# Kernel optimization log

Hardware: AMD Instinct MI355X
Metric: run time of the kernel (lower is better)

The kernel has to match this reference:

```python
import jax, jax.numpy as jnp
import numpy as np
import math

B, D, S, H = 4, 1024, 2048, 16


def setup_inputs() -> dict:
    key = jax.random.key(0)
    ks = jax.random.split(key, 9)
    scale = 0.02
    return {
        "x": jax.random.normal(ks[0], (B, D, S), dtype=jnp.float32),
        "Wq": jax.random.normal(ks[1], (D, D), dtype=jnp.float32) * scale,
        "bq": jnp.zeros((D,), dtype=jnp.float32),
        "Wk": jax.random.normal(ks[2], (D, D), dtype=jnp.float32) * scale,
        "bk": jnp.zeros((D,), dtype=jnp.float32),
        "Wv": jax.random.normal(ks[3], (D, D), dtype=jnp.float32) * scale,
        "bv": jnp.zeros((D,), dtype=jnp.float32),
        "Wo": jax.random.normal(ks[4], (D, D), dtype=jnp.float32) * scale,
        "bo": jnp.zeros((D,), dtype=jnp.float32),
        "num_heads": H,
    }


def _positional_encoding(d_model, seq_len):
    # pe[0::2, :] = sin(pos * denom), pe[1::2, :] = cos(pos * denom)
    pos = jnp.arange(seq_len, dtype=jnp.float32)[None, :]            # [1, S]
    denom = jnp.exp(jnp.arange(0, d_model, 2, dtype=jnp.float32)
                    * (-math.log(10000.0) / d_model))[:, None]        # [D/2, 1]
    angles = pos * denom                                              # [D/2, S]
    pe = jnp.zeros((d_model, seq_len), dtype=jnp.float32)
    pe = pe.at[0::2, :].set(jnp.sin(angles))
    pe = pe.at[1::2, :].set(jnp.cos(angles))
    return pe


def reference(x, Wq, bq, Wk, bk, Wv, bv, Wo, bo, num_heads):
    b, d_model, s = x.shape
    head_dim = d_model // num_heads
    x = x + _positional_encoding(d_model, s)[None, :, :]  # broadcast over batch
    x = jnp.transpose(x, (0, 2, 1))                       # [B, S, D]
    q = x @ Wq.T + bq
    k = x @ Wk.T + bk
    v = x @ Wv.T + bv
    # [B, S, H, hd] -> [B, H, S, hd]
    q = q.reshape(b, s, num_heads, head_dim).transpose(0, 2, 1, 3)
    k = k.reshape(b, s, num_heads, head_dim).transpose(0, 2, 1, 3)
    v = v.reshape(b, s, num_heads, head_dim).transpose(0, 2, 1, 3)
    scores = jnp.einsum('bhqd,bhkd->bhqk', q, k) / jnp.sqrt(
        jnp.asarray(head_dim, dtype=jnp.float32))
    attn = jax.nn.softmax(scores, axis=-1)
    out = jnp.einsum('bhqk,bhkd->bhqd', attn, v)          # [B, H, S, hd]
    out = out.transpose(0, 2, 1, 3).reshape(b, s, d_model)
    out = out @ Wo.T + bo
    return jnp.transpose(out, (0, 2, 1))                  # [B, D, S]
```

## Files before the change

kernel.cpp:

```cpp
#include <hip/hip_runtime.h>


typedef __bf16 bf16;
typedef __attribute__((ext_vector_type(8))) __bf16 bf16x8;
typedef __attribute__((ext_vector_type(4))) __bf16 bf16x4;
typedef __attribute__((ext_vector_type(4))) float f32x4;

#define NB 4
#define ND 1024
#define NS 2048
#define NH 16
#define NM 8192

__device__ __forceinline__ void gld16(const void* g, void* l) {
  __builtin_amdgcn_global_load_lds((__attribute__((address_space(1))) void*)g,
                                   (__attribute__((address_space(3))) void*)l, 16, 0, 0);
}

__device__ __forceinline__ float exp2_fast(float x) {
#if __has_builtin(__builtin_amdgcn_exp2f)
  return __builtin_amdgcn_exp2f(x);
#else
  return exp2f(x);
#endif
}

__global__ __launch_bounds__(256) void prep_x_kernel(const float* __restrict__ x,
                                                     bf16* __restrict__ xT) {
  __shared__ float t[32][33];
  const int tx = threadIdx.x, ty = threadIdx.y;
  const int s0 = blockIdx.x * 32, d0 = blockIdx.y * 32, b = blockIdx.z;
#pragma unroll
  for (int i = 0; i < 4; ++i) {
    const int rr = ty + i * 8;
    const int d = d0 + rr, s = s0 + tx;
    const float freq = __expf(-(float)(d >> 1) * 0.01798894603980689f);
    const float ang = (float)s * freq;
    const float pe = (d & 1) ? cosf(ang) : sinf(ang);
    t[rr][tx] = x[((size_t)b * ND + d) * NS + s] + pe;
  }
  __syncthreads();
#pragma unroll
  for (int i = 0; i < 4; ++i) {
    const int a = ty + i * 8;
    xT[((size_t)b * NS + s0 + a) * ND + d0 + tx] = (bf16)t[tx][a];
  }
}

__global__ __launch_bounds__(256) void prep_w_kernel(const float* __restrict__ Wq,
                                                     const float* __restrict__ Wk,
                                                     const float* __restrict__ Wv,
                                                     const float* __restrict__ Wo,
                                                     bf16* __restrict__ Wqkv,
                                                     bf16* __restrict__ WoB) {
  const size_t t = (size_t)blockIdx.x * blockDim.x + threadIdx.x;
  const size_t i = t * 4;
  const float* src;
  bf16* dst;
  size_t off;
  if (i < (size_t)3 * 1024 * 1024) {
    const int sel = (int)(i >> 20);
    src = sel == 0 ? Wq : (sel == 1 ? Wk : Wv);
    off = i - ((size_t)sel << 20);
    dst = Wqkv + i;
  } else {
    src = Wo;
    off = i - ((size_t)3 << 20);
    dst = WoB + off;
  }
  const f32x4 v = *(const f32x4*)(src + off);
  bf16x4 o;
  o[0] = (bf16)v[0];
  o[1] = (bf16)v[1];
  o[2] = (bf16)v[2];
  o[3] = (bf16)v[3];
  *(bf16x4*)dst = o;
}

__device__ __forceinline__ void gemm_tile_128(const bf16* __restrict__ A,
                                              const bf16* __restrict__ Bm,
                                              int tm, int tn, bf16* ldsA, bf16* ldsB,
                                              f32x4 acc[4][4]) {
  const int tid = threadIdx.x;
  const int lane = tid & 63, wave = tid >> 6;
  const int wm = wave >> 1, wn = wave & 1;
  const int rl = lane & 15, quad = lane >> 4;
  int r0[4], c0[4];
#pragma unroll
  for (int j = 0; j < 4; ++j) {
    const int o = (wave * 4 + j) * 1024 + lane * 16;
    const int r = o >> 7;
    r0[j] = r;
    c0[j] = ((((o >> 4) & 7) ^ (r & 7)) * 8);
  }
  for (int kt = 0; kt < 1024; kt += 64) {
#pragma unroll
    for (int j = 0; j < 4; ++j) {
      gld16(A + (size_t)(tm + r0[j]) * 1024 + kt + c0[j], (char*)ldsA + (wave * 4 + j) * 1024);
      gld16(Bm + (size_t)(tn + r0[j]) * 1024 + kt + c0[j], (char*)ldsB + (wave * 4 + j) * 1024);
    }
    __syncthreads();
#pragma unroll
    for (int kk = 0; kk < 2; ++kk) {
      bf16x8 af[4], bfr[4];
#pragma unroll
      for (int i = 0; i < 4; ++i) {
        const int ra = wm * 64 + i * 16 + rl;
        af[i] = *(const bf16x8*)((const char*)ldsA + ra * 128 +
                                 (((kk * 4 + quad) ^ (rl & 7)) * 16));
        const int rb = wn * 64 + i * 16 + rl;
        bfr[i] = *(const bf16x8*)((const char*)ldsB + rb * 128 +
                                  (((kk * 4 + quad) ^ (rl & 7)) * 16));
      }
#pragma unroll
      for (int i = 0; i < 4; ++i)
#pragma unroll
        for (int j = 0; j < 4; ++j)
          acc[i][j] =
              __builtin_amdgcn_mfma_f32_16x16x32_bf16(af[i], bfr[j], acc[i][j], 0, 0, 0);
    }
    __syncthreads();
  }
}

__global__ __launch_bounds__(256, 2) void gemm_qkv_kernel(
    const bf16* __restrict__ xT, const bf16* __restrict__ Wqkv,
    const float* __restrict__ bq, const float* __restrict__ bk,
    const float* __restrict__ bv, bf16* __restrict__ Q, bf16* __restrict__ Kb,
    bf16* __restrict__ VT) {
  __shared__ bf16 ldsA[128 * 64], ldsB[128 * 64];
  const int tm = blockIdx.x * 128, tn = blockIdx.y * 128;
  f32x4 acc[4][4];
  const f32x4 z = {0.f, 0.f, 0.f, 0.f};
#pragma unroll
  for (int i = 0; i < 4; ++i)
#pragma unroll
    for (int j = 0; j < 4; ++j) acc[i][j] = z;
  gemm_tile_128(xT, Wqkv, tm, tn, ldsA, ldsB, acc);
  const int lane = threadIdx.x & 63, wave = threadIdx.x >> 6;
  const int wm = wave >> 1, wn = wave & 1;
  const int rl = lane & 15, quad = lane >> 4;
  const float QSCALE = 0.18033688011112042f;
#pragma unroll
  for (int j = 0; j < 4; ++j) {
    const int n = tn + wn * 64 + j * 16 + rl;
    const int which = n >> 10;
    const int nl = n & 1023;
    const int h = nl >> 6, d = nl & 63;
    const float bias = (which == 0 ? bq : which == 1 ? bk : bv)[nl];
#pragma unroll
    for (int i = 0; i < 4; ++i) {
      const int m0 = tm + wm * 64 + i * 16 + quad * 4;
      const int b = m0 >> 11, s0 = m0 & 2047;
      const size_t bh = (size_t)(b * 16 + h);
      if (which == 2) {
        bf16x4 pk;
#pragma unroll
        for (int r = 0; r < 4; ++r) pk[r] = (bf16)(acc[i][j][r] + bias);
        *(bf16x4*)(VT + ((size_t)bh * 64 + d) * 2048 + s0) = pk;
      } else {
#pragma unroll
        for (int r = 0; r < 4; ++r) {
          const float v = acc[i][j][r] + bias;
          const int s = s0 + r;
          if (which == 0)
            Q[(bh * 2048 + s) * 64 + d] = (bf16)(v * QSCALE);
          else
            Kb[(bh * 2048 + s) * 64 + d] = (bf16)v;
        }
      }
    }
  }
}

__global__ __launch_bounds__(256, 2) void attn_kernel(const bf16* __restrict__ Q,
                                                      const bf16* __restrict__ Kb,
                                                      const bf16* __restrict__ VT,
                                                      bf16* __restrict__ AO) {
  __shared__ __align__(16) char smem[65536];
  char* ldsK = smem;
  char* ldsV = smem + 16384;
  char* ldsP = smem + 32768;
  const int tid = threadIdx.x;
  const int lane = tid & 63, wave = tid >> 6;
  const int rl = lane & 15, quad = lane >> 4;
  const int bh = blockIdx.x;
  const int q0 = blockIdx.y * 256;
  const bf16* Qb = Q + ((size_t)bh * 2048 + q0) * 64;
  const bf16* Kbb = Kb + (size_t)bh * 2048 * 64;
  const bf16* Vb = VT + (size_t)bh * 64 * 2048;
  const int o0 = wave * 1024 + lane * 16, o1 = o0 + 4096;
  const int ra = o0 >> 7, rb = o1 >> 7;
  const int ca = (((o0 >> 4) & 7) ^ (ra & 7)) * 16;
  const int cb = (((o1 >> 4) & 7) ^ (rb & 7)) * 16;
  gld16((const char*)Kbb + (size_t)ra * 128 + ca, ldsK + wave * 1024);
  gld16((const char*)Kbb + (size_t)rb * 128 + cb, ldsK + wave * 1024 + 4096);
  gld16((const char*)Vb + (size_t)ra * 4096 + ca, ldsV + wave * 1024);
  gld16((const char*)Vb + (size_t)rb * 4096 + cb, ldsV + wave * 1024 + 4096);
  bf16x8 qf[4][2];
#pragma unroll
  for (int i = 0; i < 4; ++i)
#pragma unroll
    for (int ks = 0; ks < 2; ++ks)
      qf[i][ks] =
          *(const bf16x8*)(Qb + (wave * 64 + i * 16 + rl) * 64 + ks * 32 + quad * 8);
  f32x4 o_acc[4][4], lacc[4];
  const f32x4 z = {0.f, 0.f, 0.f, 0.f};
#pragma unroll
  for (int i = 0; i < 4; ++i) {
    lacc[i] = z;
#pragma unroll
    for (int j = 0; j < 4; ++j) o_acc[i][j] = z;
  }
  const bf16 oneb = (bf16)1.0f;
  const bf16x8 onesb = {oneb, oneb, oneb, oneb, oneb, oneb, oneb, oneb};
  char* Pw = ldsP + wave * 8192;
  int buf = 0;
  for (int kt = 0; kt < 2048; kt += 64, buf ^= 1) {
    __syncthreads();
    if (kt + 64 < 2048) {
      const int nb = (buf ^ 1) * 8192;
      gld16((const char*)Kbb + (size_t)(kt + 64 + ra) * 128 + ca, ldsK + nb + wave * 1024);
      gld16((const char*)Kbb + (size_t)(kt + 64 + rb) * 128 + cb,
            ldsK + nb + wave * 1024 + 4096);
      gld16((const char*)Vb + (size_t)ra * 4096 + (size_t)(kt + 64) * 2 + ca,
            ldsV + nb + wave * 1024);
      gld16((const char*)Vb + (size_t)rb * 4096 + (size_t)(kt + 64) * 2 + cb,
            ldsV + nb + wave * 1024 + 4096);
    }
    const char* Kbase = ldsK + buf * 8192;
    const char* Vbase = ldsV + buf * 8192;
#pragma unroll
    for (int jk = 0; jk < 4; ++jk) {
      const bf16x8 kf0 =
          *(const bf16x8*)(Kbase + (jk * 16 + rl) * 128 + ((quad ^ (rl & 7)) * 16));
      const bf16x8 kf1 =
          *(const bf16x8*)(Kbase + (jk * 16 + rl) * 128 + (((4 + quad) ^ (rl & 7)) * 16));
#pragma unroll
      for (int i = 0; i < 4; ++i) {
        f32x4 s = z;
        s = __builtin_amdgcn_mfma_f32_16x16x32_bf16(kf0, qf[i][0], s, 0, 0, 0);
        s = __builtin_amdgcn_mfma_f32_16x16x32_bf16(kf1, qf[i][1], s, 0, 0, 0);
        bf16x4 pk;
#pragma unroll
        for (int r = 0; r < 4; ++r) pk[r] = (bf16)exp2_fast(s[r]);
        *(bf16x4*)(Pw + (i * 16 + rl) * 128 + (((jk * 2 + (quad >> 1)) ^ (rl & 7)) * 16) +
                   (quad & 1) * 8) = pk;
      }
    }
    asm volatile("s_waitcnt lgkmcnt(0)" ::: "memory");
#pragma unroll
    for (int ks = 0; ks < 2; ++ks) {
      bf16x8 pf[4];
#pragma unroll
      for (int i = 0; i < 4; ++i)
        pf[i] = *(const bf16x8*)(Pw + (i * 16 + rl) * 128 +
                                 (((ks * 4 + quad) ^ (rl & 7)) * 16));
#pragma unroll
      for (int i = 0; i < 4; ++i)
        lacc[i] = __builtin_amdgcn_mfma_f32_16x16x32_bf16(pf[i], onesb, lacc[i], 0, 0, 0);
#pragma unroll
      for (int j = 0; j < 4; ++j) {
        const bf16x8 vf = *(const bf16x8*)(Vbase + (j * 16 + rl) * 128 +
                                           (((ks * 4 + quad) ^ (rl & 7)) * 16));
#pragma unroll
        for (int i = 0; i < 4; ++i)
          o_acc[i][j] =
              __builtin_amdgcn_mfma_f32_16x16x32_bf16(pf[i], vf, o_acc[i][j], 0, 0, 0);
      }
    }
  }
  const int b = bh >> 4, h = bh & 15;
#pragma unroll
  for (int i = 0; i < 4; ++i) {
    f32x4 linv;
#pragma unroll
    for (int r = 0; r < 4; ++r) linv[r] = __builtin_amdgcn_rcpf(lacc[i][r]);
#pragma unroll
    for (int j = 0; j < 4; ++j)
#pragma unroll
      for (int r = 0; r < 4; ++r) {
        const int s = q0 + wave * 64 + i * 16 + quad * 4 + r;
        const int d = h * 64 + j * 16 + rl;
        AO[((size_t)b * 2048 + s) * 1024 + d] = (bf16)(o_acc[i][j][r] * linv[r]);
      }
  }
}

__global__ __launch_bounds__(256, 2) void gemm_out_kernel(const bf16* __restrict__ AO,
                                                          const bf16* __restrict__ WoB,
                                                          const float* __restrict__ bo,
                                                          float* __restrict__ out) {
  __shared__ bf16 ldsA[128 * 64], ldsB[128 * 64];
  const int tm = blockIdx.x * 128, tn = blockIdx.y * 128;
  f32x4 acc[4][4];
  const f32x4 z = {0.f, 0.f, 0.f, 0.f};
#pragma unroll
  for (int i = 0; i < 4; ++i)
#pragma unroll
    for (int j = 0; j < 4; ++j) acc[i][j] = z;
  gemm_tile_128(AO, WoB, tm, tn, ldsA, ldsB, acc);
  const int lane = threadIdx.x & 63, wave = threadIdx.x >> 6;
  const int wm = wave >> 1, wn = wave & 1;
  const int rl = lane & 15, quad = lane >> 4;
#pragma unroll
  for (int j = 0; j < 4; ++j) {
    const int n = tn + wn * 64 + j * 16 + rl;
    const float bias = bo[n];
#pragma unroll
    for (int i = 0; i < 4; ++i) {
      const int m0 = tm + wm * 64 + i * 16 + quad * 4;
      const int b = m0 >> 11, s = m0 & 2047;
      f32x4 v = acc[i][j];
      v[0] += bias;
      v[1] += bias;
      v[2] += bias;
      v[3] += bias;
      *(f32x4*)(out + ((size_t)(b * 1024 + n)) * 2048 + s) = v;
    }
  }
}

extern "C" void kernel_launch(void* const* d_in, const int* in_sizes, int n_in,
                              void* d_out, int out_size, void* d_ws, size_t ws_size,
                              hipStream_t stream) {
  const float* x = (const float*)d_in[0];
  const float* Wq = (const float*)d_in[1];
  const float* bq = (const float*)d_in[2];
  const float* Wk = (const float*)d_in[3];
  const float* bk = (const float*)d_in[4];
  const float* Wv = (const float*)d_in[5];
  const float* bv = (const float*)d_in[6];
  const float* Wo = (const float*)d_in[7];
  const float* bo = (const float*)d_in[8];
  float* out = (float*)d_out;

  char* p = (char*)d_ws;
  bf16* xT = (bf16*)p;
  p += (size_t)NM * ND * 2;
  bf16* Wqkv = (bf16*)p;
  p += (size_t)3 * ND * ND * 2;
  bf16* WoB = (bf16*)p;
  p += (size_t)ND * ND * 2;
  bf16* Qb = (bf16*)p;
  p += (size_t)NM * ND * 2;
  bf16* Kbf = (bf16*)p;
  p += (size_t)NM * ND * 2;
  bf16* VTb = (bf16*)p;
  p += (size_t)NM * ND * 2;
  bf16* AO = xT;

  prep_x_kernel<<<dim3(NS / 32, ND / 32, NB), dim3(32, 8), 0, stream>>>(x, xT);
  prep_w_kernel<<<dim3(4096), dim3(256), 0, stream>>>(Wq, Wk, Wv, Wo, Wqkv, WoB);
  gemm_qkv_kernel<<<dim3(NM / 128, 3072 / 128), dim3(256), 0, stream>>>(
      xT, Wqkv, bq, bk, bv, Qb, Kbf, VTb);
  attn_kernel<<<dim3(NB * NH, NS / 256), dim3(256), 0, stream>>>(Qb, Kbf, VTb, AO);
  gemm_out_kernel<<<dim3(NM / 128, ND / 128), dim3(256), 0, stream>>>(AO, WoB, bo, out);
}
```

Baseline: 278.9 us.

## Keep attention P in registers via permlane swaps and halve query tile

The attention kernel no longer writes exp'd scores to LDS and reads them back as MFMA A-operands. It builds the P fragments in registers using permlane32/permlane16 swaps, with a shuffle fallback. This drops the 32KB P buffer and the lgkmcnt wait. The query tile per block is halved to 128 rows (32 per wave) and launch bounds are raised to 4 blocks per CU, aiming for higher occupancy with less LDS. The trade-off is that K/V tiles are reloaded by twice as many blocks, and each wave does less MFMA work per K/V load.

```diff
diff --git a/kernel.cpp b/kernel.cpp
--- a/kernel.cpp
+++ b/kernel.cpp
@@ -4,7 +4,10 @@
 typedef __bf16 bf16;
 typedef __attribute__((ext_vector_type(8))) __bf16 bf16x8;
 typedef __attribute__((ext_vector_type(4))) __bf16 bf16x4;
+typedef __attribute__((ext_vector_type(2))) __bf16 bf16x2;
 typedef __attribute__((ext_vector_type(4))) float f32x4;
+typedef __attribute__((ext_vector_type(2))) unsigned int uintx2;
+typedef __attribute__((ext_vector_type(4))) unsigned int uintx4;
 
 #define NB 4
 #define ND 1024
@@ -22,6 +25,33 @@
   return __builtin_amdgcn_exp2f(x);
 #else
   return exp2f(x);
+#endif
+}
+
+__device__ __forceinline__ unsigned pk2(float a, float b) {
+  bf16x2 t;
+  t[0] = (bf16)a;
+  t[1] = (bf16)b;
+  return __builtin_bit_cast(unsigned int, t);
+}
+
+__device__ __forceinline__ void lane_xchg(unsigned a, unsigned b, unsigned& lo,
+                                          unsigned& hi) {
+#if __has_builtin(__builtin_amdgcn_permlane32_swap) && \
+    __has_builtin(__builtin_amdgcn_permlane16_swap)
+  uintx2 r = __builtin_amdgcn_permlane32_swap(a, b, false, false);
+  uintx2 r2 = __builtin_amdgcn_permlane16_swap(r[0], r[1], false, false);
+  lo = r2[0];
+  hi = r2[1];
+#else
+  const int lane = threadIdx.x & 63;
+  const int src = (lane & 15) + ((lane >> 4) & 1) * 32;
+  const unsigned as = (unsigned)__shfl((int)a, src, 64);
+  const unsigned bs = (unsigned)__shfl((int)b, src, 64);
+  const unsigned as2 = (unsigned)__shfl((int)a, src + 16, 64);
+  const unsigned bs2 = (unsigned)__shfl((int)b, src + 16, 64);
+  lo = (lane >= 32) ? bs : as;
+  hi = (lane >= 32) ? bs2 : as2;
 #endif
 }
 
@@ -173,19 +203,18 @@
   }
 }
 
-__global__ __launch_bounds__(256, 2) void attn_kernel(const bf16* __restrict__ Q,
+__global__ __launch_bounds__(256, 4) void attn_kernel(const bf16* __restrict__ Q,
                                                       const bf16* __restrict__ Kb,
                                                       const bf16* __restrict__ VT,
                                                       bf16* __restrict__ AO) {
-  __shared__ __align__(16) char smem[65536];
+  __shared__ __align__(16) char smem[32768];
   char* ldsK = smem;
   char* ldsV = smem + 16384;
-  char* ldsP = smem + 32768;
   const int tid = threadIdx.x;
   const int lane = tid & 63, wave = tid >> 6;
   const int rl = lane & 15, quad = lane >> 4;
   const int bh = blockIdx.x;
-  const int q0 = blockIdx.y * 256;
+  const int q0 = blockIdx.y * 128;
   const bf16* Qb = Q + ((size_t)bh * 2048 + q0) * 64;
   const bf16* Kbb = Kb + (size_t)bh * 2048 * 64;
   const bf16* Vb = VT + (size_t)bh * 64 * 2048;
@@ -197,24 +226,23 @@
   gld16((const char*)Kbb + (size_t)rb * 128 + cb, ldsK + wave * 1024 + 4096);
   gld16((const char*)Vb + (size_t)ra * 4096 + ca, ldsV + wave * 1024);
   gld16((const char*)Vb + (size_t)rb * 4096 + cb, ldsV + wave * 1024 + 4096);
-  bf16x8 qf[4][2];
-#pragma unroll
-  for (int i = 0; i < 4; ++i)
+  bf16x8 qf[2][2];
+#pragma unroll
+  for (int i = 0; i < 2; ++i)
 #pragma unroll
     for (int ks = 0; ks < 2; ++ks)
       qf[i][ks] =
-          *(const bf16x8*)(Qb + (wave * 64 + i * 16 + rl) * 64 + ks * 32 + quad * 8);
-  f32x4 o_acc[4][4], lacc[4];
+          *(const bf16x8*)(Qb + (wave * 32 + i * 16 + rl) * 64 + ks * 32 + quad * 8);
+  f32x4 o_acc[2][4], lacc[2];
   const f32x4 z = {0.f, 0.f, 0.f, 0.f};
 #pragma unroll
-  for (int i = 0; i < 4; ++i) {
+  for (int i = 0; i < 2; ++i) {
     lacc[i] = z;
 #pragma unroll
     for (int j = 0; j < 4; ++j) o_acc[i][j] = z;
   }
   const bf16 oneb = (bf16)1.0f;
   const bf16x8 onesb = {oneb, oneb, oneb, oneb, oneb, oneb, oneb, oneb};
-  char* Pw = ldsP + wave * 8192;
   int buf = 0;
   for (int kt = 0; kt < 2048; kt += 64, buf ^= 1) {
     __syncthreads();
@@ -231,40 +259,46 @@
     const char* Kbase = ldsK + buf * 8192;
     const char* Vbase = ldsV + buf * 8192;
 #pragma unroll
-    for (int jk = 0; jk < 4; ++jk) {
-      const bf16x8 kf0 =
-          *(const bf16x8*)(Kbase + (jk * 16 + rl) * 128 + ((quad ^ (rl & 7)) * 16));
-      const bf16x8 kf1 =
-          *(const bf16x8*)(Kbase + (jk * 16 + rl) * 128 + (((4 + quad) ^ (rl & 7)) * 16));
-#pragma unroll
-      for (int i = 0; i < 4; ++i) {
-        f32x4 s = z;
-        s = __builtin_amdgcn_mfma_f32_16x16x32_bf16(kf0, qf[i][0], s, 0, 0, 0);
-        s = __builtin_amdgcn_mfma_f32_16x16x32_bf16(kf1, qf[i][1], s, 0, 0, 0);
-        bf16x4 pk;
-#pragma unroll
-        for (int r = 0; r < 4; ++r) pk[r] = (bf16)exp2_fast(s[r]);
-        *(bf16x4*)(Pw + (i * 16 + rl) * 128 + (((jk * 2 + (quad >> 1)) ^ (rl & 7)) * 16) +
-                   (quad & 1) * 8) = pk;
-      }
-    }
-    asm volatile("s_waitcnt lgkmcnt(0)" ::: "memory");
-#pragma unroll
     for (int ks = 0; ks < 2; ++ks) {
-      bf16x8 pf[4];
-#pragma unroll
-      for (int i = 0; i < 4; ++i)
-        pf[i] = *(const bf16x8*)(Pw + (i * 16 + rl) * 128 +
-                                 (((ks * 4 + quad) ^ (rl & 7)) * 16));
-#pragma unroll
-      for (int i = 0; i < 4; ++i)
-        lacc[i] = __builtin_amdgcn_mfma_f32_16x16x32_bf16(pf[i], onesb, lacc[i], 0, 0, 0);
+      const int jk0 = ks * 2, jk1 = ks * 2 + 1;
+      const bf16x8 k00 =
+          *(const bf16x8*)(Kbase + (jk0 * 16 + rl) * 128 + ((quad ^ (rl & 7)) * 16));
+      const bf16x8 k01 =
+          *(const bf16x8*)(Kbase + (jk0 * 16 + rl) * 128 + (((4 + quad) ^ (rl & 7)) * 16));
+      const bf16x8 k10 =
+          *(const bf16x8*)(Kbase + (jk1 * 16 + rl) * 128 + ((quad ^ (rl & 7)) * 16));
+      const bf16x8 k11 =
+          *(const bf16x8*)(Kbase + (jk1 * 16 + rl) * 128 + (((4 + quad) ^ (rl & 7)) * 16));
+      bf16x8 pf[2];
+#pragma unroll
+      for (int i = 0; i < 2; ++i) {
+        f32x4 s0 = z, s1 = z;
+        s0 = __builtin_amdgcn_mfma_f32_16x16x32_bf16(k00, qf[i][0], s0, 0, 0, 0);
+        s0 = __builtin_amdgcn_mfma_f32_16x16x32_bf16(k01, qf[i][1], s0, 0, 0, 0);
+        s1 = __builtin_amdgcn_mfma_f32_16x16x32_bf16(k10, qf[i][0], s1, 0, 0, 0);
+        s1 = __builtin_amdgcn_mfma_f32_16x16x32_bf16(k11, qf[i][1], s1, 0, 0, 0);
+        const unsigned a0 = pk2(exp2_fast(s0[0]), exp2_fast(s0[1]));
+        const unsigned a1 = pk2(exp2_fast(s0[2]), exp2_fast(s0[3]));
+        const unsigned b0 = pk2(exp2_fast(s1[0]), exp2_fast(s1[1]));
+        const unsigned b1 = pk2(exp2_fast(s1[2]), exp2_fast(s1[3]));
+        unsigned d0, d1, d2, d3;
+        lane_xchg(a0, b0, d0, d2);
+        lane_xchg(a1, b1, d1, d3);
+        uintx4 dd;
+        dd[0] = d0;
+        dd[1] = d1;
+        dd[2] = d2;
+        dd[3] = d3;
+        pf[i] = __builtin_bit_cast(bf16x8, dd);
+        lacc[i] =
+            __builtin_amdgcn_mfma_f32_16x16x32_bf16(pf[i], onesb, lacc[i], 0, 0, 0);
+      }
 #pragma unroll
       for (int j = 0; j < 4; ++j) {
         const bf16x8 vf = *(const bf16x8*)(Vbase + (j * 16 + rl) * 128 +
                                            (((ks * 4 + quad) ^ (rl & 7)) * 16));
 #pragma unroll
-        for (int i = 0; i < 4; ++i)
+        for (int i = 0; i < 2; ++i)
           o_acc[i][j] =
               __builtin_amdgcn_mfma_f32_16x16x32_bf16(pf[i], vf, o_acc[i][j], 0, 0, 0);
       }
@@ -272,7 +306,7 @@
   }
   const int b = bh >> 4, h = bh & 15;
 #pragma unroll
-  for (int i = 0; i < 4; ++i) {
+  for (int i = 0; i < 2; ++i) {
     f32x4 linv;
 #pragma unroll
     for (int r = 0; r < 4; ++r) linv[r] = __builtin_amdgcn_rcpf(lacc[i][r]);
@@ -280,7 +314,7 @@
     for (int j = 0; j < 4; ++j)
 #pragma unroll
       for (int r = 0; r < 4; ++r) {
-        const int s = q0 + wave * 64 + i * 16 + quad * 4 + r;
+        const int s = q0 + wave * 32 + i * 16 + quad * 4 + r;
         const int d = h * 64 + j * 16 + rl;
         AO[((size_t)b * 2048 + s) * 1024 + d] = (bf16)(o_acc[i][j][r] * linv[r]);
       }
@@ -354,6 +388,6 @@
   prep_w_kernel<<<dim3(4096), dim3(256), 0, stream>>>(Wq, Wk, Wv, Wo, Wqkv, WoB);
   gemm_qkv_kernel<<<dim3(NM / 128, 3072 / 128), dim3(256), 0, stream>>>(
       xT, Wqkv, bq, bk, bv, Qb, Kbf, VTb);
-  attn_kernel<<<dim3(NB * NH, NS / 256), dim3(256), 0, stream>>>(Qb, Kbf, VTb, AO);
+  attn_kernel<<<dim3(NB * NH, NS / 128), dim3(256), 0, stream>>>(Qb, Kbf, VTb, AO);
   gemm_out_kernel<<<dim3(NM / 128, ND / 128), dim3(256), 0, stream>>>(AO, WoB, bo, out);
 }
```

Measured after the change: 266.5 us. 1.05x faster.
